# Performance work log

Hardware: AMD Instinct MI355X
Metric: run time of the kernel (lower is better)

## Reference

```python
import jax, jax.numpy as jnp
import numpy as np

B, T, S, C = 16, 2048, 512, 192
NEG = -1e9  # large-negative stand-in for float32.min (avoids overflow when accumulated)


def setup_inputs() -> dict:
    key = jax.random.key(0)
    ks = jax.random.split(key, 6)
    m_p = jax.random.normal(ks[0], (B, S, C), jnp.float32)
    logs_p = jax.random.normal(ks[1], (B, S, C), jnp.float32) * 0.1
    z_p = jax.random.normal(ks[2], (B, T, C), jnp.float32)
    logs_q = jax.random.normal(ks[3], (B, T, C), jnp.float32) * 0.1
    textlen = jax.random.randint(ks[4], (B,), S // 2, S + 1, jnp.int32)
    mellen = jax.random.randint(ks[5], (B,), T // 2, T + 1, jnp.int32)
    return dict(m_p=m_p, logs_p=logs_p, z_p=z_p, logs_q=logs_q,
                textlen=textlen, mellen=mellen)


def monotonic_alignment_search(ll, textlen, mellen):
    """Viterbi-style monotonic alignment. ll: [B, T, S] -> attn [B, T, S]."""
    Bb, Tt, Ss = ll.shape
    s_range = jnp.arange(Ss)
    ll_t = jnp.transpose(ll, (1, 0, 2))  # [T, B, S]

    def fwd(prob, xt):
        t, ll_row = xt
        prev = jnp.concatenate([jnp.full((Bb, 1), NEG, ll.dtype), prob[:, :-1]], axis=1)
        stay = prob >= prev  # True: best path stays at same text index
        prob = jnp.where(s_range[None] <= t, jnp.maximum(prob, prev) + ll_row, NEG)
        return prob, stay

    _, direction = jax.lax.scan(fwd, jnp.zeros((Bb, Ss), ll.dtype),
                                (jnp.arange(Tt), ll_t))  # direction: [T, B, S] bool

    def bwd(idx, xt):
        t, dir_t = xt
        active = t < mellen  # [B]
        onehot = (s_range[None] == idx[:, None]) & active[:, None]  # [B, S]
        stay = jnp.take_along_axis(dir_t, idx[:, None], axis=1)[:, 0]
        new_idx = jnp.where(active, idx - (1 - stay.astype(jnp.int32)), idx)
        return new_idx, onehot

    _, attn_rev = jax.lax.scan(bwd, textlen - 1,
                               (jnp.arange(Tt - 1, -1, -1), direction[::-1]))
    attn = attn_rev[::-1].astype(ll.dtype)  # [T, B, S]
    return jnp.transpose(attn, (1, 0, 2))


def reference(m_p, logs_p, z_p, logs_q, textlen, mellen):
    tmask = (jnp.arange(S)[None] < textlen[:, None]).astype(jnp.float32)  # [B, S]
    mmask = (jnp.arange(T)[None] < mellen[:, None]).astype(jnp.float32)   # [B, T]
    attnmask = mmask[:, :, None] * tmask[:, None]                          # [B, T, S]

    # Negative cross-entropy score matrix [B, T, S]
    s_sq_r = jnp.exp(-2.0 * logs_p)  # [B, S, C]
    nc1 = jnp.sum(-0.5 * np.log(2.0 * np.pi) - logs_p, axis=-1)[:, None]  # [B, 1, S]
    nc2 = jnp.einsum('btc,bsc->bts', -0.5 * z_p ** 2, s_sq_r)
    nc3 = jnp.einsum('btc,bsc->bts', z_p, m_p * s_sq_r)
    nc4 = jnp.sum(-0.5 * m_p ** 2 * s_sq_r, axis=-1)[:, None]             # [B, 1, S]
    neg_cent = nc1 + nc2 + nc3 + nc4

    ll = jnp.where(attnmask > 0, neg_cent, NEG)
    attn = jax.lax.stop_gradient(monotonic_alignment_search(ll, textlen, mellen))

    # Expand text-level stats to frame level via the hard alignment
    m_e = jnp.einsum('bts,bsc->btc', attn, m_p)
    l_e = jnp.einsum('bts,bsc->btc', attn, logs_p)

    kl = l_e - logs_q - 0.5 + 0.5 * (z_p - m_e) ** 2 * jnp.exp(-2.0 * l_e)
    kl = jnp.sum(kl * mmask[..., None]) / jnp.sum(mmask)
    return kl, attn
```

## Files before the change

### kernel.cpp

```cpp
#include <hip/hip_runtime.h>

#define NEGV (-1e9f)

static const int B_ = 16;
static const int T_ = 2048;
static const int S_ = 512;
static const int C_ = 192;

typedef unsigned short ushort_t;
using f32x4 = __attribute__((ext_vector_type(4))) float;
using s16x8 = __attribute__((ext_vector_type(8))) short;

__device__ __forceinline__ void split2(float x, ushort_t& h, ushort_t& l) {
    __bf16 hb = (__bf16)x;
    h = __builtin_bit_cast(ushort_t, hb);
    float r = x - (float)hb;
    __bf16 lb = (__bf16)r;
    l = __builtin_bit_cast(ushort_t, lb);
}

__global__ __launch_bounds__(256)
void prep_kernel(const float* __restrict__ m_p, const float* __restrict__ logs_p,
                 ushort_t* __restrict__ Bh, ushort_t* __restrict__ Bl,
                 float* __restrict__ nc14) {
    int wid = (blockIdx.x * blockDim.x + threadIdx.x) >> 6;
    int lane = threadIdx.x & 63;
    if (wid >= B_ * S_) return;
    const float HALF_LOG_2PI = 0.9189385332046727f;
    const float* mrow = m_p    + (size_t)wid * C_;
    const float* lrow = logs_p + (size_t)wid * C_;
    ushort_t* bh = Bh + (size_t)wid * 384;
    ushort_t* bl = Bl + (size_t)wid * 384;
    float tot = 0.f;
#pragma unroll
    for (int q = 0; q < 3; ++q) {
        int c = lane + q * 64;
        float m  = mrow[c];
        float lp = lrow[c];
        float s2r = __expf(-2.f * lp);
        float a = m * s2r;
        ushort_t h, l;
        split2(a, h, l);   bh[c] = h;        bl[c] = l;
        split2(s2r, h, l); bh[192 + c] = h;  bl[192 + c] = l;
        tot += (-HALF_LOG_2PI - lp) + (-0.5f * m * m * s2r);
    }
#pragma unroll
    for (int off = 32; off > 0; off >>= 1) tot += __shfl_xor(tot, off);
    if (lane == 0) nc14[wid] = tot;
}

#define LDP 40
__global__ __launch_bounds__(256)
void gemm_kernel(const float* __restrict__ z_p,
                 const ushort_t* __restrict__ Bh, const ushort_t* __restrict__ Bl,
                 const float* __restrict__ nc14,
                 const int* __restrict__ textlen, const int* __restrict__ mellen,
                 float* __restrict__ ll) {
    __shared__ ushort_t sAh[128 * LDP];
    __shared__ ushort_t sAl[128 * LDP];
    __shared__ ushort_t sBh[128 * LDP];
    __shared__ ushort_t sBl[128 * LDP];

    const int b  = blockIdx.z;
    const int t0 = blockIdx.y * 128;
    const int s0 = blockIdx.x * 128;
    const int tid = threadIdx.x;
    const int lane = tid & 63;
    const int wave = tid >> 6;
    const int wr = wave >> 1, wc = wave & 1;
    const int srow = tid >> 1;
    const int cb = (tid & 1) * 16;

    f32x4 acc[4][4];
#pragma unroll
    for (int m = 0; m < 4; ++m)
#pragma unroll
        for (int n = 0; n < 4; ++n) acc[m][n] = (f32x4){0.f, 0.f, 0.f, 0.f};

    const int r15 = lane & 15;
    const int klane = (lane >> 4) * 8;

    for (int kk = 0; kk < 12; ++kk) {
        {
            const int ck = (kk < 6 ? kk * 32 : (kk - 6) * 32) + cb;
            const float* src = z_p + ((size_t)b * T_ + t0 + srow) * C_ + ck;
            float e[16];
            *(float4*)(e + 0)  = *(const float4*)(src + 0);
            *(float4*)(e + 4)  = *(const float4*)(src + 4);
            *(float4*)(e + 8)  = *(const float4*)(src + 8);
            *(float4*)(e + 12) = *(const float4*)(src + 12);
            if (kk >= 6) {
#pragma unroll
                for (int i = 0; i < 16; ++i) e[i] = -0.5f * e[i] * e[i];
            }
            ushort_t h[16], l[16];
#pragma unroll
            for (int i = 0; i < 16; ++i) split2(e[i], h[i], l[i]);
            ushort_t* dh = &sAh[srow * LDP + cb];
            ushort_t* dl = &sAl[srow * LDP + cb];
            *(uint4*)dh = make_uint4(h[0] | (h[1] << 16), h[2] | (h[3] << 16),
                                     h[4] | (h[5] << 16), h[6] | (h[7] << 16));
            *(uint4*)(dh + 8) = make_uint4(h[8] | (h[9] << 16), h[10] | (h[11] << 16),
                                           h[12] | (h[13] << 16), h[14] | (h[15] << 16));
            *(uint4*)dl = make_uint4(l[0] | (l[1] << 16), l[2] | (l[3] << 16),
                                     l[4] | (l[5] << 16), l[6] | (l[7] << 16));
            *(uint4*)(dl + 8) = make_uint4(l[8] | (l[9] << 16), l[10] | (l[11] << 16),
                                           l[12] | (l[13] << 16), l[14] | (l[15] << 16));
        }
        {
            const size_t off = ((size_t)b * S_ + s0 + srow) * 384 + kk * 32 + cb;
            const uint4 u0 = *(const uint4*)(Bh + off);
            const uint4 u1 = *(const uint4*)(Bh + off + 8);
            const uint4 v0 = *(const uint4*)(Bl + off);
            const uint4 v1 = *(const uint4*)(Bl + off + 8);
            ushort_t* dh = &sBh[srow * LDP + cb];
            ushort_t* dl = &sBl[srow * LDP + cb];
            *(uint4*)dh = u0; *(uint4*)(dh + 8) = u1;
            *(uint4*)dl = v0; *(uint4*)(dl + 8) = v1;
        }
        __syncthreads();

        s16x8 ah[4], al[4], bhf[4], blf[4];
#pragma unroll
        for (int m = 0; m < 4; ++m) {
            const int row = wr * 64 + m * 16 + r15;
            ah[m] = *(const s16x8*)&sAh[row * LDP + klane];
            al[m] = *(const s16x8*)&sAl[row * LDP + klane];
        }
#pragma unroll
        for (int n = 0; n < 4; ++n) {
            const int row = wc * 64 + n * 16 + r15;
            bhf[n] = *(const s16x8*)&sBh[row * LDP + klane];
            blf[n] = *(const s16x8*)&sBl[row * LDP + klane];
        }
#pragma unroll
        for (int m = 0; m < 4; ++m)
#pragma unroll
            for (int n = 0; n < 4; ++n) {
                acc[m][n] = __builtin_amdgcn_mfma_f32_16x16x32_bf16(ah[m], bhf[n], acc[m][n], 0, 0, 0);
                acc[m][n] = __builtin_amdgcn_mfma_f32_16x16x32_bf16(ah[m], blf[n], acc[m][n], 0, 0, 0);
                acc[m][n] = __builtin_amdgcn_mfma_f32_16x16x32_bf16(al[m], bhf[n], acc[m][n], 0, 0, 0);
            }
        __syncthreads();
    }

    const int ml = mellen[b], tl = textlen[b];
    int scol[4]; float ncv[4];
#pragma unroll
    for (int n = 0; n < 4; ++n) {
        scol[n] = s0 + wc * 64 + n * 16 + r15;
        ncv[n] = nc14[b * S_ + scol[n]];
    }
#pragma unroll
    for (int m = 0; m < 4; ++m) {
        const int tb = t0 + wr * 64 + m * 16 + (lane >> 4) * 4;
#pragma unroll
        for (int r = 0; r < 4; ++r) {
            const int t = tb + r;
            const bool tm = (t < ml);
            float* orow = ll + ((size_t)b * T_ + t) * S_;
#pragma unroll
            for (int n = 0; n < 4; ++n)
                orow[scol[n]] = (tm && scol[n] < tl) ? (acc[m][n][r] + ncv[n]) : NEGV;
        }
    }
}

__global__ __launch_bounds__(64)
void mas_forward(const float* __restrict__ ll, unsigned char* __restrict__ dir) {
    const int b = blockIdx.x;
    const int lane = threadIdx.x;
    const float* llb = ll + (size_t)b * T_ * S_ + lane * 8;
    unsigned char* db = dir + ((size_t)b * T_) * 64 + lane;
    const int sbase = lane * 8;

    float4 pre[8][2];
#pragma unroll
    for (int r = 0; r < 8; ++r) {
        pre[r][0] = *(const float4*)(llb + (size_t)r * S_);
        pre[r][1] = *(const float4*)(llb + (size_t)r * S_ + 4);
    }

    float p[8];
#pragma unroll
    for (int j = 0; j < 8; ++j) p[j] = 0.f;
    float carry = (lane == 0) ? NEGV : 0.f;

    auto step = [&](int t, int ph, bool masked) {
        float cur[8];
        cur[0] = pre[ph][0].x; cur[1] = pre[ph][0].y;
        cur[2] = pre[ph][0].z; cur[3] = pre[ph][0].w;
        cur[4] = pre[ph][1].x; cur[5] = pre[ph][1].y;
        cur[6] = pre[ph][1].z; cur[7] = pre[ph][1].w;
        const int tn = t + 8;
        if (tn < T_) {
            pre[ph][0] = *(const float4*)(llb + (size_t)tn * S_);
            pre[ph][1] = *(const float4*)(llb + (size_t)tn * S_ + 4);
        }
        float v7 = fmaxf(p[7], p[6]) + cur[7];
        float nc7 = masked ? ((sbase + 7 <= t) ? v7 : NEGV) : v7;
        float newcarry = __shfl_up(nc7, 1);

        unsigned bits = (p[0] >= carry) ? 1u : 0u;
#pragma unroll
        for (int j = 1; j < 8; ++j)
            bits |= (p[j] >= p[j - 1] ? 1u : 0u) << j;

        float nv[8];
        nv[0] = fmaxf(p[0], carry) + cur[0];
#pragma unroll
        for (int j = 1; j < 7; ++j) nv[j] = fmaxf(p[j], p[j - 1]) + cur[j];
        nv[7] = v7;
        if (masked) {
#pragma unroll
            for (int j = 0; j < 8; ++j)
                p[j] = (sbase + j <= t) ? nv[j] : NEGV;
        } else {
#pragma unroll
            for (int j = 0; j < 8; ++j) p[j] = nv[j];
        }
        carry = (lane == 0) ? NEGV : newcarry;
        db[(size_t)t * 64] = (unsigned char)bits;
    };

    for (int to = 0; to < S_ / 8; ++to) {
#pragma unroll
        for (int ph = 0; ph < 8; ++ph) step(to * 8 + ph, ph, true);
    }
    for (int to = S_ / 8; to < T_ / 8; ++to) {
#pragma unroll
        for (int ph = 0; ph < 8; ++ph) step(to * 8 + ph, ph, false);
    }
}

__global__ __launch_bounds__(64)
void mas_backward(const unsigned char* __restrict__ dir,
                  const int* __restrict__ textlen, const int* __restrict__ mellen,
                  int* __restrict__ idx_arr) {
    const int b = blockIdx.x;
    const int lane = threadIdx.x;
    const int tl = textlen[b], ml = mellen[b];
    for (int t = ml + lane; t < T_; t += 64) idx_arr[b * T_ + t] = -1;
    const unsigned char* db = dir + (size_t)b * T_ * 64;
    int idx = tl - 1;
    int t_hi = ml - 1;
    while (t_hi >= 0) {
        const int lo = idx - 7;
        const int blo = (lo > 0 ? lo : 0) >> 3;
        const int bhi = idx >> 3;
        const int t = t_hi - lane;
        unsigned v = 0;
        if (lane < 8 && t >= 0) {
            unsigned b0 = db[(size_t)t * 64 + blo];
            unsigned b1 = db[(size_t)t * 64 + bhi];
            v = b0 | (b1 << 8);
        }
        unsigned vk[8];
#pragma unroll
        for (int k = 0; k < 8; ++k) vk[k] = __shfl((int)v, k);
        int emit = -1;
#pragma unroll
        for (int k = 0; k < 8; ++k) {
            const int tt = t_hi - k;
            if (tt < 0) break;
            if (lane == k) emit = idx;
            const int sb = idx >> 3;
            const unsigned byte = (sb == bhi) ? (vk[k] >> 8) : (vk[k] & 0xffu);
            const int stay = (byte >> (idx & 7)) & 1;
            idx -= (1 - stay);
            if (idx < 0) idx = 0;
        }
        const int tt = t_hi - lane;
        if (lane < 8 && tt >= 0) idx_arr[b * T_ + tt] = emit;
        t_hi -= 8;
    }
}

__global__ __launch_bounds__(256)
void scatter_attn(const int* __restrict__ idx_arr, float* __restrict__ attn) {
    const int f = blockIdx.x * blockDim.x + threadIdx.x;
    if (f >= B_ * T_) return;
    const int idx = idx_arr[f];
    if (idx >= 0) attn[(size_t)f * S_ + idx] = 1.0f;
}

__global__ __launch_bounds__(256)
void kl_frames(const float* __restrict__ m_p, const float* __restrict__ logs_p,
               const float* __restrict__ z_p, const float* __restrict__ logs_q,
               const int* __restrict__ idx_arr, const int* __restrict__ mellen,
               float* __restrict__ frame_kl) {
    const int wid = (blockIdx.x * blockDim.x + threadIdx.x) >> 6;
    const int lane = threadIdx.x & 63;
    if (wid >= B_ * T_) return;
    const int b = wid >> 11;
    const int t = wid & (T_ - 1);
    const int ml = mellen[b];
    float total = 0.f;
    if (t < ml) {
        const int idx = idx_arr[wid];
        const float* mr = m_p    + ((size_t)b * S_ + idx) * C_;
        const float* lr = logs_p + ((size_t)b * S_ + idx) * C_;
        const float* zr = z_p    + (size_t)wid * C_;
        const float* qr = logs_q + (size_t)wid * C_;
#pragma unroll
        for (int q = 0; q < 3; ++q) {
            const int c = lane + q * 64;
            const float le = lr[c];
            const float d = zr[c] - mr[c];
            total += le - qr[c] - 0.5f + 0.5f * d * d * __expf(-2.f * le);
        }
    }
#pragma unroll
    for (int off = 32; off > 0; off >>= 1) total += __shfl_xor(total, off);
    if (lane == 0) frame_kl[wid] = total;
}

__global__ __launch_bounds__(256)
void kl_reduce(const float* __restrict__ frame_kl, const int* __restrict__ mellen,
               float* __restrict__ out) {
    __shared__ float sm[256];
    const int tid = threadIdx.x;
    float s = 0.f;
    for (int k = tid; k < B_ * T_; k += 256) s += frame_kl[k];
    sm[tid] = s;
    __syncthreads();
    for (int off = 128; off > 0; off >>= 1) {
        if (tid < off) sm[tid] += sm[tid + off];
        __syncthreads();
    }
    if (tid == 0) {
        int sum_ml = 0;
        for (int bq = 0; bq < B_; ++bq) sum_ml += mellen[bq];
        out[0] = sm[0] / (float)sum_ml;
    }
}

extern "C" void kernel_launch(void* const* d_in, const int* in_sizes, int n_in,
                              void* d_out, int out_size, void* d_ws, size_t ws_size,
                              hipStream_t stream) {
    const float* m_p    = (const float*)d_in[0];
    const float* logs_p = (const float*)d_in[1];
    const float* z_p    = (const float*)d_in[2];
    const float* logs_q = (const float*)d_in[3];
    const int*   textlen = (const int*)d_in[4];
    const int*   mellen  = (const int*)d_in[5];

    float* out = (float*)d_out;
    float* attn = out + 1;
    float* ll = attn;

    char* ws = (char*)d_ws;
    const size_t OFF_BH   = 0;
    const size_t OFF_BL   = OFF_BH + (size_t)B_ * S_ * 384 * 2;
    const size_t OFF_NC   = OFF_BL + (size_t)B_ * S_ * 384 * 2;
    const size_t OFF_DIR  = OFF_NC + (size_t)B_ * S_ * 4;
    const size_t OFF_IDX  = OFF_DIR + (size_t)B_ * T_ * 64;
    const size_t OFF_FKL  = OFF_IDX + (size_t)B_ * T_ * 4;
    ushort_t* Bh = (ushort_t*)(ws + OFF_BH);
    ushort_t* Bl = (ushort_t*)(ws + OFF_BL);
    float* nc14 = (float*)(ws + OFF_NC);
    unsigned char* dir = (unsigned char*)(ws + OFF_DIR);
    int* idx_arr = (int*)(ws + OFF_IDX);
    float* frame_kl = (float*)(ws + OFF_FKL);

    prep_kernel<<<(B_ * S_) / 4, 256, 0, stream>>>(m_p, logs_p, Bh, Bl, nc14);
    gemm_kernel<<<dim3(S_ / 128, T_ / 128, B_), 256, 0, stream>>>(
        z_p, Bh, Bl, nc14, textlen, mellen, ll);
    mas_forward<<<B_, 64, 0, stream>>>(ll, dir);
    mas_backward<<<B_, 64, 0, stream>>>(dir, textlen, mellen, idx_arr);
    hipMemsetAsync(attn, 0, (size_t)B_ * T_ * S_ * 4, stream);
    scatter_attn<<<(B_ * T_ + 255) / 256, 256, 0, stream>>>(idx_arr, attn);
    kl_frames<<<(B_ * T_) / 4, 256, 0, stream>>>(m_p, logs_p, z_p, logs_q,
                                                 idx_arr, mellen, frame_kl);
    kl_reduce<<<1, 256, 0, stream>>>(frame_kl, mellen, out);
}
```

Baseline: 509.2 us.

## Pipeline MAS forward across four wavefronts with LDS boundary handoff

The Viterbi forward pass now uses four wavefronts per batch instead of one. Each wavefront owns 128 text columns and each lane holds two cells instead of eight, so the serial per-step chain gets shorter. Each wavefront publishes its last-column values per time step into shared memory along with a progress counter. The next wavefront spin-waits on that counter, which turns the column split into a wavefront pipeline. This adds skew, spin-wait synchronisation through volatile LDS, and extra shuffles to pack the direction bits.

```diff
diff --git a/kernel.cpp b/kernel.cpp
--- a/kernel.cpp
+++ b/kernel.cpp
@@ -166,70 +166,90 @@
     }
 }
 
-__global__ __launch_bounds__(64)
+__global__ __launch_bounds__(256)
 void mas_forward(const float* __restrict__ ll, unsigned char* __restrict__ dir) {
+    __shared__ float val[3][T_];
+    __shared__ int prog[3];
     const int b = blockIdx.x;
-    const int lane = threadIdx.x;
-    const float* llb = ll + (size_t)b * T_ * S_ + lane * 8;
-    unsigned char* db = dir + ((size_t)b * T_) * 64 + lane;
-    const int sbase = lane * 8;
-
-    float4 pre[8][2];
-#pragma unroll
-    for (int r = 0; r < 8; ++r) {
-        pre[r][0] = *(const float4*)(llb + (size_t)r * S_);
-        pre[r][1] = *(const float4*)(llb + (size_t)r * S_ + 4);
-    }
-
-    float p[8];
-#pragma unroll
-    for (int j = 0; j < 8; ++j) p[j] = 0.f;
-    float carry = (lane == 0) ? NEGV : 0.f;
-
-    auto step = [&](int t, int ph, bool masked) {
-        float cur[8];
-        cur[0] = pre[ph][0].x; cur[1] = pre[ph][0].y;
-        cur[2] = pre[ph][0].z; cur[3] = pre[ph][0].w;
-        cur[4] = pre[ph][1].x; cur[5] = pre[ph][1].y;
-        cur[6] = pre[ph][1].z; cur[7] = pre[ph][1].w;
-        const int tn = t + 8;
-        if (tn < T_) {
-            pre[ph][0] = *(const float4*)(llb + (size_t)tn * S_);
-            pre[ph][1] = *(const float4*)(llb + (size_t)tn * S_ + 4);
-        }
-        float v7 = fmaxf(p[7], p[6]) + cur[7];
-        float nc7 = masked ? ((sbase + 7 <= t) ? v7 : NEGV) : v7;
-        float newcarry = __shfl_up(nc7, 1);
-
-        unsigned bits = (p[0] >= carry) ? 1u : 0u;
-#pragma unroll
-        for (int j = 1; j < 8; ++j)
-            bits |= (p[j] >= p[j - 1] ? 1u : 0u) << j;
-
-        float nv[8];
-        nv[0] = fmaxf(p[0], carry) + cur[0];
-#pragma unroll
-        for (int j = 1; j < 7; ++j) nv[j] = fmaxf(p[j], p[j - 1]) + cur[j];
-        nv[7] = v7;
-        if (masked) {
-#pragma unroll
-            for (int j = 0; j < 8; ++j)
-                p[j] = (sbase + j <= t) ? nv[j] : NEGV;
+    const int tid = threadIdx.x;
+    const int w = tid >> 6;
+    const int lane = tid & 63;
+    if (tid < 3) prog[tid] = 0;
+    __syncthreads();
+
+    volatile int* vprog = prog;
+    volatile float* vval = &val[0][0];
+
+    const int wbase = w * 128;
+    const int s0 = wbase + lane * 2;
+    const float* llw = ll + (size_t)b * T_ * S_ + s0;
+    unsigned char* db = dir + (size_t)b * T_ * 64 + w * 16 + (lane >> 2);
+    const bool storer = (lane & 3) == 0;
+    const bool prod = (w < 3) && (lane == 63);
+
+    float2 pre[8];
+#pragma unroll
+    for (int r = 0; r < 8; ++r)
+        pre[r] = *(const float2*)(llw + (size_t)(wbase + r) * S_);
+
+    float p0 = (w == 0) ? 0.f : NEGV;
+    float p1 = p0;
+
+    auto group = [&](int g, const float* lv, bool masked) {
+        const int t8 = g * 8;
+#pragma unroll
+        for (int ph = 0; ph < 8; ++ph) {
+            const int t = t8 + ph;
+            float2 cur = pre[ph];
+            const int tn = t + 8;
+            if (tn < T_) pre[ph] = *(const float2*)(llw + (size_t)tn * S_);
+
+            float prev0 = __shfl_up(p1, 1);
+            if (lane == 0) prev0 = lv[ph];
+
+            unsigned bits2 = ((p0 >= prev0) ? 1u : 0u) | ((p1 >= p0) ? 2u : 0u);
+
+            float v0 = fmaxf(p0, prev0) + cur.x;
+            float v1 = fmaxf(p1, p0) + cur.y;
+            if (masked) {
+                p0 = (s0 <= t) ? v0 : NEGV;
+                p1 = (s0 + 1 <= t) ? v1 : NEGV;
+            } else {
+                p0 = v0;
+                p1 = v1;
+            }
+
+            unsigned tp = bits2 | (__shfl_xor((int)bits2, 1) << 2);
+            tp = tp | (__shfl_xor((int)tp, 2) << 4);
+            if (storer) db[(size_t)t * 64] = (unsigned char)tp;
+            if (prod) vval[w * T_ + t] = p1;
+        }
+        if (prod) vprog[w] = t8 + 8;
+    };
+
+    auto fetch_lv = [&](int g, float* lv) {
+        if (w > 0) {
+            const int need = g * 8 + 8;
+            while (vprog[w - 1] < need) {}
+#pragma unroll
+            for (int i = 0; i < 8; ++i)
+                lv[i] = vval[(w - 1) * T_ + g * 8 - 1 + i];
         } else {
 #pragma unroll
-            for (int j = 0; j < 8; ++j) p[j] = nv[j];
-        }
-        carry = (lane == 0) ? NEGV : newcarry;
-        db[(size_t)t * 64] = (unsigned char)bits;
+            for (int i = 0; i < 8; ++i) lv[i] = NEGV;
+        }
     };
 
-    for (int to = 0; to < S_ / 8; ++to) {
-#pragma unroll
-        for (int ph = 0; ph < 8; ++ph) step(to * 8 + ph, ph, true);
-    }
-    for (int to = S_ / 8; to < T_ / 8; ++to) {
-#pragma unroll
-        for (int ph = 0; ph < 8; ++ph) step(to * 8 + ph, ph, false);
+    const int g0 = wbase >> 3;
+    for (int g = g0; g < g0 + 16; ++g) {
+        float lv[8];
+        fetch_lv(g, lv);
+        group(g, lv, true);
+    }
+    for (int g = g0 + 16; g < T_ / 8; ++g) {
+        float lv[8];
+        fetch_lv(g, lv);
+        group(g, lv, false);
     }
 }
 
@@ -303,7 +323,7 @@
         const float* zr = z_p    + (size_t)wid * C_;
         const float* qr = logs_q + (size_t)wid * C_;
 #pragma unroll
-        for (int q = 0; q < 3; ++q) {
+    for (int q = 0; q < 3; ++q) {
             const int c = lane + q * 64;
             const float le = lr[c];
             const float d = zr[c] - mr[c];
@@ -366,7 +386,7 @@
     prep_kernel<<<(B_ * S_) / 4, 256, 0, stream>>>(m_p, logs_p, Bh, Bl, nc14);
     gemm_kernel<<<dim3(S_ / 128, T_ / 128, B_), 256, 0, stream>>>(
         z_p, Bh, Bl, nc14, textlen, mellen, ll);
-    mas_forward<<<B_, 64, 0, stream>>>(ll, dir);
+    mas_forward<<<B_, 256, 0, stream>>>(ll, dir);
     mas_backward<<<B_, 64, 0, stream>>>(dir, textlen, mellen, idx_arr);
     hipMemsetAsync(attn, 0, (size_t)B_ * T_ * S_ * 4, stream);
     scatter_attn<<<(B_ * T_ + 255) / 256, 256, 0, stream>>>(idx_arr, attn);
```

New measurement: 1.027 ms. 2.02x slower.
